# Optimization experiments

Hardware: AMD Instinct MI355X
Metric: run time of the kernel (lower is better)

## Reference

```python
import jax, jax.numpy as jnp
import numpy as np

VOCAB = 50000
D = 256
NUM_GROUPS = 2
NUM_BEAMS = 4
MAX_LEN = 24
DIV_STRENGTH = 0.5


def setup_inputs() -> dict:
    key = jax.random.key(0)
    k1, k2, k3, k4 = jax.random.split(key, 4)
    B, S = 8, 128
    src = jax.random.normal(k1, (B, S, D), jnp.float32)
    We = jax.random.normal(k2, (D, D), jnp.float32) * (1.0 / np.sqrt(D))
    Emb = jax.random.normal(k3, (VOCAB, D), jnp.float32) * 0.02
    Wout = jax.random.normal(k4, (D, VOCAB), jnp.float32) * (1.0 / np.sqrt(D))
    return {"src": src, "We": We, "Emb": Emb, "Wout": Wout}


def _beam_search(src, We, Emb, Wout):
    B = src.shape[0]
    K, V, L = NUM_BEAMS, VOCAB, MAX_LEN

    # encoder: linear projection; decoder context = mean-pooled encoder output
    enc_out = jnp.einsum('bsd,de->bse', src, We)      # [B, S, D]
    ctx = enc_out.mean(axis=1)                        # [B, D]
    ctx_rep = jnp.repeat(ctx, K, axis=0)              # [B*K, D]
    beam_ids = jnp.arange(K)[:, None, None]           # [K,1,1]

    all_seqs, all_scores = [], []
    for g in range(NUM_GROUPS):
        prev = jnp.stack(all_seqs) if g > 0 else None  # [g, B, K, L]

        def step(carry, t, prev=prev):
            seqs, gs = carry                           # [B,K,L] int32, [B,K] f32
            tok = jax.lax.dynamic_index_in_dim(seqs, t - 1, axis=2, keepdims=False)  # [B,K]
            h = Emb[tok.reshape(-1)] + ctx_rep         # [B*K, D]
            logits = h @ Wout                          # [B*K, V]
            scores = jax.nn.log_softmax(logits, axis=-1).reshape(B, K, V)
            if prev is not None:
                # diversity penalty: subtract strength once per token present
                # anywhere (any batch, pos < t) in prev group's beam b (unique() semantics)
                posmask = (jnp.arange(L) < t).astype(scores.dtype)   # [L]
                w = jnp.broadcast_to(posmask, (K, B, L))

                def presence(pseq):                    # pseq: [B,K,L]
                    tok_t = pseq.transpose(1, 0, 2)    # [K,B,L]
                    cnt = jnp.zeros((K, V), scores.dtype).at[beam_ids, tok_t].add(w)
                    return (cnt > 0).astype(scores.dtype)

                pen = jax.vmap(presence)(prev).sum(axis=0)           # [K,V]
                scores = scores - DIV_STRENGTH * pen[None, :, :]
            total = (gs[:, :, None] + scores).reshape(B, K * V)
            topk_scores, topk_idx = jax.lax.top_k(total, K)          # [B,K]
            beam_idx = topk_idx // V
            next_tok = topk_idx % V
            seqs = jnp.take_along_axis(seqs, beam_idx[:, :, None], axis=1)
            seqs = seqs.at[:, :, t].set(next_tok)
            return (seqs, topk_scores), None

        init_scores = jnp.full((B, K), -1e9, jnp.float32).at[:, 0].set(0.0)
        init_seqs = jnp.zeros((B, K, L), jnp.int32).at[:, :, 0].set(1)  # BOS=1
        (seqs, gscores), _ = jax.lax.scan(step, (init_seqs, init_scores), jnp.arange(1, L))
        all_seqs.append(seqs)
        all_scores.append(gscores)

    return jnp.concatenate(all_seqs, axis=1), jnp.concatenate(all_scores, axis=1)


def reference(src, We, Emb, Wout):
    # returns (final_sequences [B, G*K, L] int32, final_scores [B, G*K] f32)
    return _beam_search(src, We, Emb, Wout)
```

## Files before the change

### kernel.cpp

```cpp
#include <hip/hip_runtime.h>
#include <math.h>

#define VOCAB 50000
#define DM 256
#define NB 8
#define NK 4
#define SL 24
#define NROW 32
#define CBLK 256
#define NXB 196
#define NPART NXB
#define DIVS 0.5f
#define NCH 49
#define SCH 1024

__device__ __forceinline__ bool cbetter(float av, int ai, float bv, int bi) {
  return (av > bv) || (av == bv && ai < bi);
}

__device__ __forceinline__ void merge4(const float* av, const int* ai,
                                       const float* bv, const int* bi,
                                       float* rv, int* ri) {
  int x = 0, y = 0;
#pragma unroll
  for (int j = 0; j < 4; ++j) {
    bool ta = cbetter(av[x], ai[x], bv[y], bi[y]);
    rv[j] = ta ? av[x] : bv[y];
    ri[j] = ta ? ai[x] : bi[y];
    if (ta) ++x; else ++y;
  }
}

__global__ void k_prep(const float* __restrict__ src, const float* __restrict__ We,
                       float* __restrict__ ctx) {
  int b = blockIdx.x, d = threadIdx.x;
  __shared__ float sm[DM];
  const float* p = src + (size_t)b * 128 * DM + d;
  float s = 0.f;
  for (int i = 0; i < 128; ++i) s += p[i * DM];
  sm[d] = s * (1.f / 128.f);
  __syncthreads();
  float acc = 0.f;
  for (int dp = 0; dp < DM; ++dp) acc += sm[dp] * We[dp * DM + d];
  ctx[b * DM + d] = acc;
}

__global__ void k_eprep(const float* __restrict__ Emb, const float* __restrict__ ctx,
                        const int* __restrict__ seq, float* __restrict__ eg, int t) {
  int r = blockIdx.x, d = threadIdx.x;
  int tok = seq[r * SL + (t - 1)];
  eg[r * DM + d] = Emb[(size_t)tok * DM + d] + ctx[(r >> 2) * DM + d];
}

__global__ __launch_bounds__(512) void k_logits(
    const float* __restrict__ Wout, const float* __restrict__ eg,
    float* __restrict__ logits, float* __restrict__ pm, float* __restrict__ ps) {
  int tid = threadIdx.x;
  int lane = tid & 63, wq = tid >> 6;
  int c0 = blockIdx.x * CBLK + lane * 4;
  bool valid = (c0 + 3 < VOCAB);
  const float* wbase = Wout + (valid ? c0 : (VOCAB - 4));
  int rb = __builtin_amdgcn_readfirstlane(wq) * 4;
  const float* e0 = eg + (size_t)rb * DM;
  float acc[4][4];
#pragma unroll
  for (int r = 0; r < 4; ++r)
#pragma unroll
    for (int c = 0; c < 4; ++c) acc[r][c] = 0.f;

  for (int d = 0; d < DM; d += 8) {
    float4 w[8];
#pragma unroll
    for (int j = 0; j < 8; ++j)
      w[j] = *reinterpret_cast<const float4*>(wbase + (size_t)(d + j) * VOCAB);
#pragma unroll
    for (int r = 0; r < 4; ++r) {
      const float* ep = e0 + r * DM + d;
      const float4 ea = *reinterpret_cast<const float4*>(ep);
      const float4 eb = *reinterpret_cast<const float4*>(ep + 4);
#pragma unroll
      for (int c = 0; c < 4; ++c) {
        float a = acc[r][c];
        a = fmaf(ea.x, (&w[0].x)[c], a);
        a = fmaf(ea.y, (&w[1].x)[c], a);
        a = fmaf(ea.z, (&w[2].x)[c], a);
        a = fmaf(ea.w, (&w[3].x)[c], a);
        a = fmaf(eb.x, (&w[4].x)[c], a);
        a = fmaf(eb.y, (&w[5].x)[c], a);
        a = fmaf(eb.z, (&w[6].x)[c], a);
        a = fmaf(eb.w, (&w[7].x)[c], a);
        acc[r][c] = a;
      }
    }
  }
  if (valid) {
#pragma unroll
    for (int r = 0; r < 4; ++r) {
      float4 o = make_float4(acc[r][0], acc[r][1], acc[r][2], acc[r][3]);
      *reinterpret_cast<float4*>(&logits[(size_t)(rb + r) * VOCAB + c0]) = o;
    }
  }
#pragma unroll
  for (int r = 0; r < 4; ++r) {
    float m = valid ? fmaxf(fmaxf(acc[r][0], acc[r][1]), fmaxf(acc[r][2], acc[r][3]))
                    : -INFINITY;
#pragma unroll
    for (int o = 32; o >= 1; o >>= 1) m = fmaxf(m, __shfl_xor(m, o));
    float sv = 0.f;
    if (valid && m != -INFINITY) {
      sv = expf(acc[r][0] - m) + expf(acc[r][1] - m) +
           expf(acc[r][2] - m) + expf(acc[r][3] - m);
    }
#pragma unroll
    for (int o = 32; o >= 1; o >>= 1) sv += __shfl_xor(sv, o);
    if (lane == 0) {
      pm[(size_t)(rb + r) * NPART + blockIdx.x] = m;
      ps[(size_t)(rb + r) * NPART + blockIdx.x] = sv;
    }
  }
}

__global__ __launch_bounds__(256) void k_topk_s1(
    const float* __restrict__ logits, const float* __restrict__ pm,
    const float* __restrict__ ps, const float* __restrict__ gs_src,
    const int* __restrict__ minpos, float* __restrict__ s1v,
    int* __restrict__ s1i, int t, int g) {
  int b = blockIdx.x / NCH, c = blockIdx.x % NCH, tid = threadIdx.x;
  int lane = tid & 63, wave = tid >> 6;
  __shared__ float gsv[NK], lsev[NK];
  __shared__ float lv[256][4];
  __shared__ int li[256][4];
  if (tid < NK) gsv[tid] = gs_src[b * NK + tid];
  {
    int row = b * NK + wave;
    const float* pmr = pm + (size_t)row * NPART;
    const float* psr = ps + (size_t)row * NPART;
    float M = -INFINITY, S = 0.f;
    for (int j = lane; j < NPART; j += 64) {
      float mj = pmr[j];
      if (mj != -INFINITY) {
        float sj = psr[j];
        float Mn = fmaxf(M, mj);
        S = (M == -INFINITY) ? sj * expf(mj - Mn)
                             : S * expf(M - Mn) + sj * expf(mj - Mn);
        M = Mn;
      }
    }
#pragma unroll
    for (int o = 32; o >= 1; o >>= 1) {
      float Mo = __shfl_xor(M, o);
      float So = __shfl_xor(S, o);
      if (Mo != -INFINITY) {
        float Mn = fmaxf(M, Mo);
        S = (M == -INFINITY) ? So * expf(Mo - Mn)
                             : S * expf(M - Mn) + So * expf(Mo - Mn);
        M = Mn;
      }
    }
    if (lane == 0) lsev[wave] = M + logf(S);
  }
  __syncthreads();

  float tv[4]; int ti[4];
#pragma unroll
  for (int j = 0; j < 4; ++j) { tv[j] = -INFINITY; ti[j] = 0x7fffffff; }

  int v = c * SCH + tid * 4;
  for (int k = 0; k < NK; ++k) {
    float gsk = gsv[k], lsek = lsev[k];
    const float* lrow = logits + (size_t)(b * NK + k) * VOCAB;
    const int* mp = minpos + (size_t)k * VOCAB;
    if (v + 3 < VOCAB) {
      float4 x4 = *reinterpret_cast<const float4*>(lrow + v);
      float xs[4] = {x4.x, x4.y, x4.z, x4.w};
      int pen[4] = {0, 0, 0, 0};
      if (g) {
        int4 m4 = *reinterpret_cast<const int4*>(mp + v);
        pen[0] = m4.x < t; pen[1] = m4.y < t; pen[2] = m4.z < t; pen[3] = m4.w < t;
      }
#pragma unroll
      for (int i = 0; i < 4; ++i) {
        float sc = xs[i] - lsek;
        if (pen[i]) sc -= DIVS;
        float x = gsk + sc;
        int idx = k * VOCAB + v + i;
        if (cbetter(x, idx, tv[3], ti[3])) {
          int pos = 3;
          if (cbetter(x, idx, tv[2], ti[2])) { tv[3]=tv[2]; ti[3]=ti[2]; pos=2;
            if (cbetter(x, idx, tv[1], ti[1])) { tv[2]=tv[1]; ti[2]=ti[1]; pos=1;
              if (cbetter(x, idx, tv[0], ti[0])) { tv[1]=tv[0]; ti[1]=ti[0]; pos=0; } } }
          tv[pos] = x; ti[pos] = idx;
        }
      }
    } else {
#pragma unroll
      for (int i = 0; i < 4; ++i) {
        int vv = v + i;
        if (vv >= VOCAB) break;
        float sc = lrow[vv] - lsek;
        if (g && mp[vv] < t) sc -= DIVS;
        float x = gsk + sc;
        int idx = k * VOCAB + vv;
        if (cbetter(x, idx, tv[3], ti[3])) {
          int pos = 3;
          if (cbetter(x, idx, tv[2], ti[2])) { tv[3]=tv[2]; ti[3]=ti[2]; pos=2;
            if (cbetter(x, idx, tv[1], ti[1])) { tv[2]=tv[1]; ti[2]=ti[1]; pos=1;
              if (cbetter(x, idx, tv[0], ti[0])) { tv[1]=tv[0]; ti[1]=ti[0]; pos=0; } } }
          tv[pos] = x; ti[pos] = idx;
        }
      }
    }
  }
#pragma unroll
  for (int j = 0; j < 4; ++j) { lv[tid][j] = tv[j]; li[tid][j] = ti[j]; }
  __syncthreads();
  for (int s = 128; s >= 1; s >>= 1) {
    if (tid < s) {
      float av[4], bv[4], rv[4]; int ai[4], bi[4], ri[4];
#pragma unroll
      for (int j = 0; j < 4; ++j) { av[j]=lv[tid][j]; ai[j]=li[tid][j]; bv[j]=lv[tid+s][j]; bi[j]=li[tid+s][j]; }
      merge4(av, ai, bv, bi, rv, ri);
#pragma unroll
      for (int j = 0; j < 4; ++j) { lv[tid][j]=rv[j]; li[tid][j]=ri[j]; }
    }
    __syncthreads();
  }
  if (tid == 0) {
#pragma unroll
    for (int j = 0; j < 4; ++j) {
      s1v[(b * NCH + c) * 4 + j] = lv[0][j];
      s1i[(b * NCH + c) * 4 + j] = li[0][j];
    }
  }
}

__global__ __launch_bounds__(256) void k_topk_s2(
    const float* __restrict__ s1v, const int* __restrict__ s1i,
    const int* __restrict__ seq_src, const float* __restrict__ Emb,
    const float* __restrict__ ctx, float* __restrict__ gs_dst,
    int* __restrict__ seq_dst, float* __restrict__ eg,
    int t, int g, float* __restrict__ out) {
  int b = blockIdx.x, tid = threadIdx.x;
  __shared__ float lv[64][4];
  __shared__ int li[64][4];
  __shared__ int oldseq[NK * SL];
  __shared__ float selv[NK];
  __shared__ int selb[NK], selt[NK];
  if (tid < 64) {
#pragma unroll
    for (int j = 0; j < 4; ++j) {
      if (tid < NCH) { lv[tid][j] = s1v[(b * NCH + tid) * 4 + j]; li[tid][j] = s1i[(b * NCH + tid) * 4 + j]; }
      else { lv[tid][j] = -INFINITY; li[tid][j] = 0x7fffffff; }
    }
  }
  if (tid < NK * SL) oldseq[tid] = seq_src[b * NK * SL + tid];
  __syncthreads();
  for (int s = 32; s >= 1; s >>= 1) {
    if (tid < s) {
      float av[4], bv[4], rv[4]; int ai[4], bi[4], ri[4];
#pragma unroll
      for (int j = 0; j < 4; ++j) { av[j]=lv[tid][j]; ai[j]=li[tid][j]; bv[j]=lv[tid+s][j]; bi[j]=li[tid+s][j]; }
      merge4(av, ai, bv, bi, rv, ri);
#pragma unroll
      for (int j = 0; j < 4; ++j) { lv[tid][j]=rv[j]; li[tid][j]=ri[j]; }
    }
    __syncthreads();
  }
  if (tid == 0) {
#pragma unroll
    for (int j = 0; j < 4; ++j) {
      selv[j] = lv[0][j];
      selb[j] = li[0][j] / VOCAB;
      selt[j] = li[0][j] % VOCAB;
    }
  }
  __syncthreads();
  if (tid < NK * SL) {
    int j = tid / SL, l = tid % SL;
    int tok = (l == t) ? selt[j] : oldseq[selb[j] * SL + l];
    seq_dst[b * NK * SL + tid] = tok;
    if (t == SL - 1) out[(size_t)b * (2 * NK * SL) + (g * NK + j) * SL + l] = (float)tok;
  }
  if (tid < NK) {
    gs_dst[b * NK + tid] = selv[tid];
    if (t == SL - 1) out[NB * 2 * NK * SL + b * (2 * NK) + g * NK + tid] = selv[tid];
  }
  if (t < SL - 1) {
    int d = tid;
#pragma unroll
    for (int j = 0; j < NK; ++j) {
      int nt_ = selt[j];
      eg[(size_t)(b * NK + j) * DM + d] = Emb[(size_t)nt_ * DM + d] + ctx[b * DM + d];
    }
  }
}

__global__ void k_init(int* __restrict__ seqA, float* __restrict__ gsA) {
  int i = threadIdx.x;
  seqA[i] = (i % SL == 0) ? 1 : 0;
  if (i < NB * NK) gsA[i] = ((i & 3) == 0) ? 0.f : -1e9f;
}

__global__ void k_minpos_init(int* __restrict__ minpos) {
  int i = blockIdx.x * 256 + threadIdx.x;
  if (i < NK * VOCAB) minpos[i] = 1 << 30;
}

__global__ void k_minpos_scatter(const int* __restrict__ seq, int* __restrict__ minpos) {
  int i = threadIdx.x;
  int l = i % SL;
  int k = (i / SL) % NK;
  int tok = seq[i];
  atomicMin(&minpos[(size_t)k * VOCAB + tok], l);
}

extern "C" void kernel_launch(void* const* d_in, const int* in_sizes, int n_in,
                              void* d_out, int out_size, void* d_ws, size_t ws_size,
                              hipStream_t stream) {
  (void)in_sizes; (void)n_in; (void)out_size; (void)ws_size;
  const float* src  = (const float*)d_in[0];
  const float* We   = (const float*)d_in[1];
  const float* Emb  = (const float*)d_in[2];
  const float* Wout = (const float*)d_in[3];
  float* out = (float*)d_out;
  char* ws = (char*)d_ws;
  size_t off = 0;
  auto carve = [&](size_t bytes) {
    char* p = ws + off;
    off += (bytes + 255) & ~(size_t)255;
    return p;
  };
  float* ctx    = (float*)carve((size_t)NB * DM * 4);
  float* eg     = (float*)carve((size_t)NROW * DM * 4);
  float* logits = (float*)carve((size_t)NROW * VOCAB * 4);
  float* pm     = (float*)carve((size_t)NROW * NPART * 4);
  float* ps     = (float*)carve((size_t)NROW * NPART * 4);
  int*   seqA   = (int*)carve((size_t)NB * NK * SL * 4);
  int*   seqB   = (int*)carve((size_t)NB * NK * SL * 4);
  float* gsA    = (float*)carve((size_t)NROW * 4);
  float* gsB    = (float*)carve((size_t)NROW * 4);
  int*   minpos = (int*)carve((size_t)NK * VOCAB * 4);
  float* s1v    = (float*)carve((size_t)NB * NCH * 4 * 4);
  int*   s1i    = (int*)carve((size_t)NB * NCH * 4 * 4);

  hipLaunchKernelGGL(k_prep, dim3(NB), dim3(DM), 0, stream, src, We, ctx);

  for (int g = 0; g < 2; ++g) {
    hipLaunchKernelGGL(k_init, dim3(1), dim3(768), 0, stream, seqA, gsA);
    for (int t = 1; t < SL; ++t) {
      int* ssrc = ((t - 1) & 1) ? seqB : seqA;
      int* sdst = (t & 1) ? seqB : seqA;
      float* gsrc = ((t - 1) & 1) ? gsB : gsA;
      float* gdst = (t & 1) ? gsB : gsA;
      if (t == 1)
        hipLaunchKernelGGL(k_eprep, dim3(NROW), dim3(DM), 0, stream,
                           Emb, ctx, ssrc, eg, t);
      hipLaunchKernelGGL(k_logits, dim3(NXB), dim3(512), 0, stream,
                         Wout, eg, logits, pm, ps);
      hipLaunchKernelGGL(k_topk_s1, dim3(NB * NCH), dim3(256), 0, stream,
                         logits, pm, ps, gsrc, minpos, s1v, s1i, t, g);
      hipLaunchKernelGGL(k_topk_s2, dim3(NB), dim3(256), 0, stream,
                         s1v, s1i, ssrc, Emb, ctx, gdst, sdst, eg, t, g, out);
    }
    if (g == 0) {
      hipLaunchKernelGGL(k_minpos_init, dim3((NK * VOCAB + 255) / 256), dim3(256), 0, stream, minpos);
      hipLaunchKernelGGL(k_minpos_scatter, dim3(1), dim3(768), 0, stream, seqB, minpos);
    }
  }
}
```

Measured before the change: 2.277 ms.

## Fuse top-k stage 2 into stage 1 via last-block atomic counter; double-buffer Wout loads

Removes the separate k_topk_s2 launch per step by having the last-finishing block of each batch in k_topk_s1, detected with an atomic counter and threadfences, perform the final merge, sequence update and embedding prep. Separately, the logits GEMV loop now double-buffers Wout float4 loads so the next 8 rows load while the current 8 are multiplied. This saves one launch per step (46 total) and aims to hide memory latency, at the cost of higher register pressure and an extra atomic per block.

```diff
diff --git a/kernel.cpp b/kernel.cpp
--- a/kernel.cpp
+++ b/kernel.cpp
@@ -52,6 +52,32 @@
   eg[r * DM + d] = Emb[(size_t)tok * DM + d] + ctx[(r >> 2) * DM + d];
 }
 
+#define FMA_BATCH(W, DBASE)                                               \
+  _Pragma("unroll")                                                       \
+  for (int r = 0; r < 4; ++r) {                                           \
+    const float* ep = e0 + r * DM + (DBASE);                              \
+    const float4 ea = *reinterpret_cast<const float4*>(ep);               \
+    const float4 eb = *reinterpret_cast<const float4*>(ep + 4);           \
+    _Pragma("unroll")                                                     \
+    for (int c = 0; c < 4; ++c) {                                         \
+      float a = acc[r][c];                                                \
+      a = fmaf(ea.x, (&W[0].x)[c], a);                                    \
+      a = fmaf(ea.y, (&W[1].x)[c], a);                                    \
+      a = fmaf(ea.z, (&W[2].x)[c], a);                                    \
+      a = fmaf(ea.w, (&W[3].x)[c], a);                                    \
+      a = fmaf(eb.x, (&W[4].x)[c], a);                                    \
+      a = fmaf(eb.y, (&W[5].x)[c], a);                                    \
+      a = fmaf(eb.z, (&W[6].x)[c], a);                                    \
+      a = fmaf(eb.w, (&W[7].x)[c], a);                                    \
+      acc[r][c] = a;                                                      \
+    }                                                                     \
+  }
+
+#define LOAD_BATCH(W, DBASE)                                              \
+  _Pragma("unroll")                                                       \
+  for (int j = 0; j < 8; ++j)                                             \
+    W[j] = *reinterpret_cast<const float4*>(wbase + (size_t)((DBASE) + j) * VOCAB);
+
 __global__ __launch_bounds__(512) void k_logits(
     const float* __restrict__ Wout, const float* __restrict__ eg,
     float* __restrict__ logits, float* __restrict__ pm, float* __restrict__ ps) {
@@ -68,31 +94,15 @@
 #pragma unroll
     for (int c = 0; c < 4; ++c) acc[r][c] = 0.f;
 
-  for (int d = 0; d < DM; d += 8) {
-    float4 w[8];
-#pragma unroll
-    for (int j = 0; j < 8; ++j)
-      w[j] = *reinterpret_cast<const float4*>(wbase + (size_t)(d + j) * VOCAB);
-#pragma unroll
-    for (int r = 0; r < 4; ++r) {
-      const float* ep = e0 + r * DM + d;
-      const float4 ea = *reinterpret_cast<const float4*>(ep);
-      const float4 eb = *reinterpret_cast<const float4*>(ep + 4);
-#pragma unroll
-      for (int c = 0; c < 4; ++c) {
-        float a = acc[r][c];
-        a = fmaf(ea.x, (&w[0].x)[c], a);
-        a = fmaf(ea.y, (&w[1].x)[c], a);
-        a = fmaf(ea.z, (&w[2].x)[c], a);
-        a = fmaf(ea.w, (&w[3].x)[c], a);
-        a = fmaf(eb.x, (&w[4].x)[c], a);
-        a = fmaf(eb.y, (&w[5].x)[c], a);
-        a = fmaf(eb.z, (&w[6].x)[c], a);
-        a = fmaf(eb.w, (&w[7].x)[c], a);
-        acc[r][c] = a;
-      }
-    }
-  }
+  float4 wA[8], wB[8];
+  LOAD_BATCH(wA, 0);
+  for (int d = 0; d < DM; d += 16) {
+    LOAD_BATCH(wB, d + 8);
+    FMA_BATCH(wA, d);
+    if (d + 16 < DM) { LOAD_BATCH(wA, d + 16); }
+    FMA_BATCH(wB, d + 8);
+  }
+
   if (valid) {
 #pragma unroll
     for (int r = 0; r < 4; ++r) {
@@ -124,7 +134,11 @@
     const float* __restrict__ logits, const float* __restrict__ pm,
     const float* __restrict__ ps, const float* __restrict__ gs_src,
     const int* __restrict__ minpos, float* __restrict__ s1v,
-    int* __restrict__ s1i, int t, int g) {
+    int* __restrict__ s1i, int* __restrict__ cnt,
+    const int* __restrict__ seq_src, const float* __restrict__ Emb,
+    const float* __restrict__ ctx, float* __restrict__ gs_dst,
+    int* __restrict__ seq_dst, float* __restrict__ eg,
+    int t, int g, float* __restrict__ out) {
   int b = blockIdx.x / NCH, c = blockIdx.x % NCH, tid = threadIdx.x;
   int lane = tid & 63, wave = tid >> 6;
   __shared__ float gsv[NK], lsev[NK];
@@ -232,17 +246,17 @@
       s1i[(b * NCH + c) * 4 + j] = li[0][j];
     }
   }
-}
-
-__global__ __launch_bounds__(256) void k_topk_s2(
-    const float* __restrict__ s1v, const int* __restrict__ s1i,
-    const int* __restrict__ seq_src, const float* __restrict__ Emb,
-    const float* __restrict__ ctx, float* __restrict__ gs_dst,
-    int* __restrict__ seq_dst, float* __restrict__ eg,
-    int t, int g, float* __restrict__ out) {
-  int b = blockIdx.x, tid = threadIdx.x;
-  __shared__ float lv[64][4];
-  __shared__ int li[64][4];
+  __shared__ int isLast;
+  __threadfence();
+  if (tid == 0) {
+    int old = atomicAdd(&cnt[b], 1);
+    isLast = (old == NCH - 1);
+  }
+  __syncthreads();
+  if (!isLast) return;
+  __threadfence();
+  if (tid == 0) cnt[b] = 0;
+
   __shared__ int oldseq[NK * SL];
   __shared__ float selv[NK];
   __shared__ int selb[NK], selt[NK];
@@ -295,10 +309,12 @@
   }
 }
 
-__global__ void k_init(int* __restrict__ seqA, float* __restrict__ gsA) {
+__global__ void k_init(int* __restrict__ seqA, float* __restrict__ gsA,
+                       int* __restrict__ cnt) {
   int i = threadIdx.x;
   seqA[i] = (i % SL == 0) ? 1 : 0;
   if (i < NB * NK) gsA[i] = ((i & 3) == 0) ? 0.f : -1e9f;
+  if (i < NB) cnt[i] = 0;
 }
 
 __global__ void k_minpos_init(int* __restrict__ minpos) {
@@ -342,11 +358,12 @@
   int*   minpos = (int*)carve((size_t)NK * VOCAB * 4);
   float* s1v    = (float*)carve((size_t)NB * NCH * 4 * 4);
   int*   s1i    = (int*)carve((size_t)NB * NCH * 4 * 4);
+  int*   cnt    = (int*)carve((size_t)NB * 4);
 
   hipLaunchKernelGGL(k_prep, dim3(NB), dim3(DM), 0, stream, src, We, ctx);
 
   for (int g = 0; g < 2; ++g) {
-    hipLaunchKernelGGL(k_init, dim3(1), dim3(768), 0, stream, seqA, gsA);
+    hipLaunchKernelGGL(k_init, dim3(1), dim3(768), 0, stream, seqA, gsA, cnt);
     for (int t = 1; t < SL; ++t) {
       int* ssrc = ((t - 1) & 1) ? seqB : seqA;
       int* sdst = (t & 1) ? seqB : seqA;
@@ -358,9 +375,8 @@
       hipLaunchKernelGGL(k_logits, dim3(NXB), dim3(512), 0, stream,
                          Wout, eg, logits, pm, ps);
       hipLaunchKernelGGL(k_topk_s1, dim3(NB * NCH), dim3(256), 0, stream,
-                         logits, pm, ps, gsrc, minpos, s1v, s1i, t, g);
-      hipLaunchKernelGGL(k_topk_s2, dim3(NB), dim3(256), 0, stream,
-                         s1v, s1i, ssrc, Emb, ctx, gdst, sdst, eg, t, g, out);
+                         logits, pm, ps, gsrc, minpos, s1v, s1i, cnt,
+                         ssrc, Emb, ctx, gdst, sdst, eg, t, g, out);
     }
     if (g == 0) {
       hipLaunchKernelGGL(k_minpos_init, dim3((NK * VOCAB + 255) / 256), dim3(256), 0, stream, minpos);
```

Result: slower. 3.875 ms (+70.2%).

## Pre-tile Wout into contiguous per-block column panels for logits GEMV

Applied to the files above, without the earlier changes.

Adds a one-time kernel that copies Wout into a block-tiled layout where each 256-column block's 256 rows sit contiguously. The logits kernel then reads each block's weights from a compact 256 KB region instead of strided rows of stride VOCAB, aiming to improve DRAM page locality and prefetch efficiency across the 46 decode steps. This costs an extra full copy of Wout per call and extra workspace, and it falls back to the old kernel if the workspace is too small.

```diff
diff --git a/kernel.cpp b/kernel.cpp
--- a/kernel.cpp
+++ b/kernel.cpp
@@ -52,7 +52,82 @@
   eg[r * DM + d] = Emb[(size_t)tok * DM + d] + ctx[(r >> 2) * DM + d];
 }
 
-__global__ __launch_bounds__(512) void k_logits(
+__global__ void k_wtile(const float* __restrict__ Wout, float* __restrict__ WT) {
+  int b = blockIdx.x, d = blockIdx.y, c = threadIdx.x;
+  int col = b * CBLK + c;
+  WT[(size_t)b * (CBLK * DM) + d * CBLK + c] =
+      (col < VOCAB) ? Wout[(size_t)d * VOCAB + col] : 0.f;
+}
+
+__global__ __launch_bounds__(512) void k_logits_tiled(
+    const float* __restrict__ WT, const float* __restrict__ eg,
+    float* __restrict__ logits, float* __restrict__ pm, float* __restrict__ ps) {
+  int tid = threadIdx.x;
+  int lane = tid & 63, wq = tid >> 6;
+  int c0 = blockIdx.x * CBLK + lane * 4;
+  bool valid = (c0 + 3 < VOCAB);
+  const float* wbase = WT + (size_t)blockIdx.x * (CBLK * DM) + lane * 4;
+  int rb = __builtin_amdgcn_readfirstlane(wq) * 4;
+  const float* e0 = eg + (size_t)rb * DM;
+  float acc[4][4];
+#pragma unroll
+  for (int r = 0; r < 4; ++r)
+#pragma unroll
+    for (int c = 0; c < 4; ++c) acc[r][c] = 0.f;
+
+  for (int d = 0; d < DM; d += 8) {
+    float4 w[8];
+#pragma unroll
+    for (int j = 0; j < 8; ++j)
+      w[j] = *reinterpret_cast<const float4*>(wbase + (size_t)(d + j) * CBLK);
+#pragma unroll
+    for (int r = 0; r < 4; ++r) {
+      const float* ep = e0 + r * DM + d;
+      const float4 ea = *reinterpret_cast<const float4*>(ep);
+      const float4 eb = *reinterpret_cast<const float4*>(ep + 4);
+#pragma unroll
+      for (int c = 0; c < 4; ++c) {
+        float a = acc[r][c];
+        a = fmaf(ea.x, (&w[0].x)[c], a);
+        a = fmaf(ea.y, (&w[1].x)[c], a);
+        a = fmaf(ea.z, (&w[2].x)[c], a);
+        a = fmaf(ea.w, (&w[3].x)[c], a);
+        a = fmaf(eb.x, (&w[4].x)[c], a);
+        a = fmaf(eb.y, (&w[5].x)[c], a);
+        a = fmaf(eb.z, (&w[6].x)[c], a);
+        a = fmaf(eb.w, (&w[7].x)[c], a);
+        acc[r][c] = a;
+      }
+    }
+  }
+  if (valid) {
+#pragma unroll
+    for (int r = 0; r < 4; ++r) {
+      float4 o = make_float4(acc[r][0], acc[r][1], acc[r][2], acc[r][3]);
+      *reinterpret_cast<float4*>(&logits[(size_t)(rb + r) * VOCAB + c0]) = o;
+    }
+  }
+#pragma unroll
+  for (int r = 0; r < 4; ++r) {
+    float m = valid ? fmaxf(fmaxf(acc[r][0], acc[r][1]), fmaxf(acc[r][2], acc[r][3]))
+                    : -INFINITY;
+#pragma unroll
+    for (int o = 32; o >= 1; o >>= 1) m = fmaxf(m, __shfl_xor(m, o));
+    float sv = 0.f;
+    if (valid && m != -INFINITY) {
+      sv = expf(acc[r][0] - m) + expf(acc[r][1] - m) +
+           expf(acc[r][2] - m) + expf(acc[r][3] - m);
+    }
+#pragma unroll
+    for (int o = 32; o >= 1; o >>= 1) sv += __shfl_xor(sv, o);
+    if (lane == 0) {
+      pm[(size_t)(rb + r) * NPART + blockIdx.x] = m;
+      ps[(size_t)(rb + r) * NPART + blockIdx.x] = sv;
+    }
+  }
+}
+
+__global__ __launch_bounds__(512) void k_logits_flat(
     const float* __restrict__ Wout, const float* __restrict__ eg,
     float* __restrict__ logits, float* __restrict__ pm, float* __restrict__ ps) {
   int tid = threadIdx.x;
@@ -67,7 +142,6 @@
   for (int r = 0; r < 4; ++r)
 #pragma unroll
     for (int c = 0; c < 4; ++c) acc[r][c] = 0.f;
-
   for (int d = 0; d < DM; d += 8) {
     float4 w[8];
 #pragma unroll
@@ -317,7 +391,7 @@
 extern "C" void kernel_launch(void* const* d_in, const int* in_sizes, int n_in,
                               void* d_out, int out_size, void* d_ws, size_t ws_size,
                               hipStream_t stream) {
-  (void)in_sizes; (void)n_in; (void)out_size; (void)ws_size;
+  (void)in_sizes; (void)n_in; (void)out_size;
   const float* src  = (const float*)d_in[0];
   const float* We   = (const float*)d_in[1];
   const float* Emb  = (const float*)d_in[2];
@@ -342,8 +416,13 @@
   int*   minpos = (int*)carve((size_t)NK * VOCAB * 4);
   float* s1v    = (float*)carve((size_t)NB * NCH * 4 * 4);
   int*   s1i    = (int*)carve((size_t)NB * NCH * 4 * 4);
+  size_t wt_bytes = (size_t)NXB * CBLK * DM * 4;
+  bool use_tile = (off + wt_bytes + 256 <= ws_size);
+  float* WT = use_tile ? (float*)carve(wt_bytes) : nullptr;
 
   hipLaunchKernelGGL(k_prep, dim3(NB), dim3(DM), 0, stream, src, We, ctx);
+  if (use_tile)
+    hipLaunchKernelGGL(k_wtile, dim3(NXB, DM), dim3(CBLK), 0, stream, Wout, WT);
 
   for (int g = 0; g < 2; ++g) {
     hipLaunchKernelGGL(k_init, dim3(1), dim3(768), 0, stream, seqA, gsA);
@@ -355,8 +434,12 @@
       if (t == 1)
         hipLaunchKernelGGL(k_eprep, dim3(NROW), dim3(DM), 0, stream,
                            Emb, ctx, ssrc, eg, t);
-      hipLaunchKernelGGL(k_logits, dim3(NXB), dim3(512), 0, stream,
-                         Wout, eg, logits, pm, ps);
+      if (use_tile)
+        hipLaunchKernelGGL(k_logits_tiled, dim3(NXB), dim3(512), 0, stream,
+                           WT, eg, logits, pm, ps);
+      else
+        hipLaunchKernelGGL(k_logits_flat, dim3(NXB), dim3(512), 0, stream,
+                           Wout, eg, logits, pm, ps);
       hipLaunchKernelGGL(k_topk_s1, dim3(NB * NCH), dim3(256), 0, stream,
                          logits, pm, ps, gsrc, minpos, s1v, s1i, t, g);
       hipLaunchKernelGGL(k_topk_s2, dim3(NB), dim3(256), 0, stream,
```

Measured after the change: 2.247 ms, median of 2. Within noise of the previous version (-1.3%).
